# Kernel tuning notes

Measured on AMD Instinct MI355X. Metric: run time of the kernel, lower is better.

## Reference

```python
import jax, jax.numpy as jnp
import numpy as np
import math

B, H, L = 8, 256, 4096
C = 1            # channels
D_STATE = 64
DD = D_STATE // 2  # d = 32
DT_MIN, DT_MAX = 1e-3, 1e-1


def setup_inputs() -> dict:
    key = jax.random.key(0)
    ks = jax.random.split(key, 6)
    u = jax.random.normal(ks[0], (B, H, L), dtype=jnp.float32)
    # analytic init matching the torch module
    h_scale = jnp.exp(jnp.arange(H, dtype=jnp.float32) / H * math.log(DT_MAX / DT_MIN))  # (H,)
    angles = jnp.arange(DD, dtype=jnp.float32) * jnp.float32(np.pi)                      # (DD,)
    theta = jnp.einsum('c,h,d->chd', jnp.ones((C,), jnp.float32), h_scale, angles)       # (C,H,DD)
    a = -jnp.broadcast_to(h_scale[None, :, None], (C, H, DD)).astype(jnp.float32)        # (C,H,DD)
    D = jax.random.normal(ks[1], (C, H), dtype=jnp.float32)
    b_p = jax.random.normal(ks[2], (C, H, DD), dtype=jnp.float32)
    c_p = jax.random.normal(ks[3], (C, H, DD), dtype=jnp.float32)
    x0 = jax.random.normal(ks[4], (C, H, DD), dtype=jnp.float32)
    return {"u": u, "theta": theta, "a": a, "D": D, "b_p": b_p, "c_p": c_p, "x0": x0}


def fft_conv(u, f):
    # u: (B,H,L), f: (C,H,L) -> (B,C,H,L) causal conv via zero-padded FFT
    l = u.shape[-1]
    n = 2 * l
    u_f = jnp.fft.rfft(u, n=n)          # (B,H,n//2+1)
    f_f = jnp.fft.rfft(f, n=n)          # (C,H,n//2+1)
    y_f = jnp.einsum('bhl,chl->bchl', u_f, f_f)
    return jnp.fft.irfft(y_f, n=n)[..., :l]


def reference(u, theta, a, D, b_p, c_p, x0):
    l = u.shape[-1]
    T = 1.0 / (l - 1)
    zk = T * jnp.arange(l, dtype=jnp.float32)            # (L,)
    zk4 = zk[None, None, :, None]                         # (1,1,L,1)
    ls = -jnp.abs(a) + 1j * theta                         # (C,H,DD) complex
    term_0 = (jnp.exp(ls * T) - 1.0) / ls                 # (C,H,DD)
    # base_term: (C,H,L,DD)
    base_term = (2.0 * term_0[:, :, None, :] * jnp.exp(ls[:, :, None, :] * zk4)).real
    q = b_p * c_p                                         # (C,H,DD)
    f = jnp.einsum('chd,chld->chl', q, base_term)         # (C,H,L)
    y = fft_conv(u, f)                                    # (B,C,H,L)
    y = y + jnp.einsum('bhl,ch->bchl', u, D)
    # initial-condition term
    cos_term = 2.0 * T * jnp.exp(-jnp.abs(a)[:, :, None, :] * zk4) * jnp.cos(theta[:, :, None, :] * zk4)
    init = jnp.einsum('chd,chld->chl', 2.0 * (c_p * x0), cos_term)  # (C,H,L)
    y = y + init[None]                                    # broadcast over batch
    b = y.shape[0]
    return y.reshape(b, -1, l)                            # (B, C*H, L)
```

## Files before the change

kernel.cpp:

```cpp
#include <hip/hip_runtime.h>

#define BB 8
#define HH 256
#define LL 4096
#define DD2 32
#define STR 72
#define ESTR 65

typedef __attribute__((ext_vector_type(8))) short short8;
typedef __attribute__((ext_vector_type(4))) float f32x4;

static __device__ inline unsigned short f2bf(float x) {
    union { float f; unsigned u; } v; v.f = x;
    unsigned r = v.u + 0x7fffu + ((v.u >> 16) & 1u);
    return (unsigned short)(r >> 16);
}

#define CMUL(or_, oi_, ar_, ai_, br_, bi_) do { \
    float _tr = fmaf((ar_), (br_), -(ai_) * (bi_)); \
    float _ti = fmaf((ar_), (bi_), (ai_) * (br_)); \
    (or_) = _tr; (oi_) = _ti; } while (0)

__global__ __launch_bounds__(256) void s4_mfma_kernel(
    const float* __restrict__ u,
    const float* __restrict__ theta,
    const float* __restrict__ a,
    const float* __restrict__ Dp,
    const float* __restrict__ b_p,
    const float* __restrict__ c_p,
    const float* __restrict__ x0,
    float* __restrict__ out)
{
    const int tid = threadIdx.x;
    const int bh  = blockIdx.x;
    const int hh  = bh & (HH - 1);
    const float T = 1.0f / (LL - 1);

    __shared__ __align__(16) short lds[18432 + 128];
    short* Us = lds;
    short* Hs = lds + 4608;
    short* Ps = lds + 9216;
    short* Rs = lds + 13824;
    float* h_s = (float*)&lds[18432];
    float* Es  = (float*)&lds[4608];

    const float* up = u + ((size_t)bh << 12);
    #pragma unroll
    for (int jj = 0; jj < 4; ++jj) {
        const int v  = tid + (jj << 8);
        const float4 val = ((const float4*)up)[v];
        const int c  = v >> 4;
        const int t0 = (v & 15) << 2;
        uint2 pk;
        pk.x = (unsigned)f2bf(val.x) | ((unsigned)f2bf(val.y) << 16);
        pk.y = (unsigned)f2bf(val.z) | ((unsigned)f2bf(val.w) << 16);
        *(uint2*)&Us[c * STR + t0] = pk;
    }

    const int d  = tid & 31;
    const int kb = tid >> 5;
    const float lr = a[hh * DD2 + d];
    const float li = theta[hh * DD2 + d];
    float sn, cS;
    sincosf(li * T, &sn, &cS);
    const float er = expf(lr * T);
    const float Rr = er * cS, Ri = er * sn;
    const float den = lr * lr + li * li;
    const float t0r = ((Rr - 1.f) * lr + Ri * li) / den;
    const float t0i = (Ri * lr - (Rr - 1.f) * li) / den;
    const float qq  = b_p[hh * DD2 + d] * c_p[hh * DD2 + d];
    const float wre = 2.f * qq * t0r, wim = 2.f * qq * t0i;
    const float vv  = 4.f * T * c_p[hh * DD2 + d] * x0[hh * DD2 + d];

    float r2r, r2i, r4r, r4i, r8r, r8i, r16r, r16i, r32r, r32i;
    CMUL(r2r, r2i, Rr, Ri, Rr, Ri);
    CMUL(r4r, r4i, r2r, r2i, r2r, r2i);
    CMUL(r8r, r8i, r4r, r4i, r4r, r4i);
    CMUL(r16r, r16i, r8r, r8i, r8r, r8i);
    CMUL(r32r, r32i, r16r, r16i, r16r, r16i);

    float pr = 1.f, pi = 0.f;
    if (kb & 1) CMUL(pr, pi, pr, pi, r8r, r8i);
    if (kb & 2) CMUL(pr, pi, pr, pi, r16r, r16i);
    if (kb & 4) CMUL(pr, pi, pr, pi, r32r, r32i);

    #pragma unroll
    for (int k8 = 0; k8 < 8; ++k8) {
        const int k = (kb << 3) + k8;
        Rs[k * STR + d]       = (short)f2bf(pr);
        Rs[k * STR + 32 + d]  = (short)f2bf(-pi);
        Ps[d * STR + (63 - k)]        = (short)f2bf(pr);
        Ps[(32 + d) * STR + (63 - k)] = (short)f2bf(pi);
        float hk = fmaf(wre, pr, -wim * pi);
        hk += __shfl_xor(hk, 1);
        hk += __shfl_xor(hk, 2);
        hk += __shfl_xor(hk, 4);
        hk += __shfl_xor(hk, 8);
        hk += __shfl_xor(hk, 16);
        if (d == 0) h_s[k] = hk;
        CMUL(pr, pi, pr, pi, Rr, Ri);
    }
    __syncthreads();

    {
        const int t  = tid >> 2;
        const int tb = (tid & 3) << 4;
        #pragma unroll
        for (int g = 0; g < 4; ++g) {
            const int tau0 = tb + (g << 2);
            unsigned short e[4];
            #pragma unroll
            for (int i = 0; i < 4; ++i) {
                const int dt = t - (tau0 + i);
                e[i] = (dt >= 0) ? f2bf(h_s[dt]) : (unsigned short)0;
            }
            uint2 pk;
            pk.x = (unsigned)e[0] | ((unsigned)e[1] << 16);
            pk.y = (unsigned)e[2] | ((unsigned)e[3] << 16);
            *(uint2*)&Hs[t * STR + tau0] = pk;
        }
    }
    __syncthreads();

    const int ln   = tid & 63;
    const int m0   = (tid >> 6) << 4;
    const int rowi = ln & 15;
    const int quad = ln >> 4;
    f32x4 accY[4], accE[4];
    #pragma unroll
    for (int nt = 0; nt < 4; ++nt) {
        accY[nt] = (f32x4){0.f, 0.f, 0.f, 0.f};
        accE[nt] = (f32x4){0.f, 0.f, 0.f, 0.f};
    }
    #pragma unroll
    for (int k0 = 0; k0 < 64; k0 += 32) {
        const short8 aH = *(const short8*)&Hs[(m0 + rowi) * STR + k0 + (quad << 3)];
        const short8 aP = *(const short8*)&Ps[(m0 + rowi) * STR + k0 + (quad << 3)];
        #pragma unroll
        for (int nt = 0; nt < 4; ++nt) {
            const short8 bU = *(const short8*)&Us[((nt << 4) + rowi) * STR + k0 + (quad << 3)];
            accY[nt] = __builtin_amdgcn_mfma_f32_16x16x32_bf16(aH, bU, accY[nt], 0, 0, 0);
            accE[nt] = __builtin_amdgcn_mfma_f32_16x16x32_bf16(aP, bU, accE[nt], 0, 0, 0);
        }
    }
    __syncthreads();

    #pragma unroll
    for (int nt = 0; nt < 4; ++nt)
        #pragma unroll
        for (int i = 0; i < 4; ++i)
            Es[(m0 + (quad << 2) + i) * ESTR + (nt << 4) + rowi] = accE[nt][i];
    __syncthreads();

    if (tid < 32) {
        float Sr = 0.f, Si = 0.f;
        float Gr = vv, Gi = 0.f;
        float Ar, Ai;
        CMUL(Ar, Ai, r32r, r32i, r32r, r32i);
        float wrrR, wrrI;
        CMUL(wrrR, wrrI, wre, wim, Rr, Ri);
        short* Qs = Us;
        for (int c = 0; c < 64; ++c) {
            const float Er = Es[d * ESTR + c];
            const float Ei = Es[(32 + d) * ESTR + c];
            const float Qr = fmaf(wrrR, Sr, fmaf(-wrrI, Si, Gr));
            const float Qi = fmaf(wrrR, Si, fmaf(wrrI, Sr, Gi));
            Qs[c * STR + d]      = (short)f2bf(Qr);
            Qs[c * STR + 32 + d] = (short)f2bf(Qi);
            const float nSr = fmaf(Ar, Sr, fmaf(-Ai, Si, Er));
            const float nSi = fmaf(Ar, Si, fmaf(Ai, Sr, Ei));
            Sr = nSr; Si = nSi;
            float nGr, nGi;
            CMUL(nGr, nGi, Ar, Ai, Gr, Gi);
            Gr = nGr; Gi = nGi;
        }
    }
    __syncthreads();

    #pragma unroll
    for (int k0 = 0; k0 < 64; k0 += 32) {
        const short8 aR = *(const short8*)&Rs[(m0 + rowi) * STR + k0 + (quad << 3)];
        #pragma unroll
        for (int nt = 0; nt < 4; ++nt) {
            const short8 bQ = *(const short8*)&Us[((nt << 4) + rowi) * STR + k0 + (quad << 3)];
            accY[nt] = __builtin_amdgcn_mfma_f32_16x16x32_bf16(aR, bQ, accY[nt], 0, 0, 0);
        }
    }

    const float Dh = Dp[hh];
    float* op = out + ((size_t)bh << 12);
    #pragma unroll
    for (int nt = 0; nt < 4; ++nt) {
        const int c    = (nt << 4) + rowi;
        const int toff = m0 + (quad << 2);
        const float4 uu = *(const float4*)&up[c * 64 + toff];
        float4 res;
        res.x = fmaf(Dh, uu.x, accY[nt][0]);
        res.y = fmaf(Dh, uu.y, accY[nt][1]);
        res.z = fmaf(Dh, uu.z, accY[nt][2]);
        res.w = fmaf(Dh, uu.w, accY[nt][3]);
        *(float4*)&op[c * 64 + toff] = res;
    }
}

extern "C" void kernel_launch(void* const* d_in, const int* in_sizes, int n_in,
                              void* d_out, int out_size, void* d_ws, size_t ws_size,
                              hipStream_t stream) {
    const float* u     = (const float*)d_in[0];
    const float* theta = (const float*)d_in[1];
    const float* a     = (const float*)d_in[2];
    const float* Dp    = (const float*)d_in[3];
    const float* b_p   = (const float*)d_in[4];
    const float* c_p   = (const float*)d_in[5];
    const float* x0    = (const float*)d_in[6];
    float* out = (float*)d_out;
    hipLaunchKernelGGL(s4_mfma_kernel, dim3(BB * HH), dim3(256), 0, stream,
                       u, theta, a, Dp, b_p, c_p, x0, out);
}
```

Measured before the change: 110.8 us.

## Parallelize chunk-state scan across all threads and shrink LDS footprint

The serial 64-step inter-chunk recurrence, which previously ran on only 32 threads, becomes a two-level scan. Each of 8 thread groups scans 8 chunks, segment sums are combined with powers of A, and each group then emits its own Q rows. The E buffer is stored as bf16 and aliased with the H buffer, and the R matrix is built later into the P region. Together these cut LDS to about 30KB, and launch bounds now request 5 blocks per CU. The u reload is also hoisted before the final MFMA, at the cost of extra bf16 rounding in the scan state and a few more syncs.

```diff
diff --git a/kernel.cpp b/kernel.cpp
--- a/kernel.cpp
+++ b/kernel.cpp
@@ -5,7 +5,8 @@
 #define LL 4096
 #define DD2 32
 #define STR 72
-#define ESTR 65
+#define ESTRS 140
+#define SEGSTR 18
 
 typedef __attribute__((ext_vector_type(8))) short short8;
 typedef __attribute__((ext_vector_type(4))) float f32x4;
@@ -15,13 +16,16 @@
     unsigned r = v.u + 0x7fffu + ((v.u >> 16) & 1u);
     return (unsigned short)(r >> 16);
 }
+static __device__ inline float bf2f(unsigned us) {
+    union { unsigned u; float f; } v; v.u = us << 16; return v.f;
+}
 
 #define CMUL(or_, oi_, ar_, ai_, br_, bi_) do { \
     float _tr = fmaf((ar_), (br_), -(ai_) * (bi_)); \
     float _ti = fmaf((ar_), (bi_), (ai_) * (br_)); \
     (or_) = _tr; (oi_) = _ti; } while (0)
 
-__global__ __launch_bounds__(256) void s4_mfma_kernel(
+__global__ __launch_bounds__(256, 5) void s4_mfma_kernel(
     const float* __restrict__ u,
     const float* __restrict__ theta,
     const float* __restrict__ a,
@@ -36,13 +40,14 @@
     const int hh  = bh & (HH - 1);
     const float T = 1.0f / (LL - 1);
 
-    __shared__ __align__(16) short lds[18432 + 128];
-    short* Us = lds;
-    short* Hs = lds + 4608;
-    short* Ps = lds + 9216;
-    short* Rs = lds + 13824;
-    float* h_s = (float*)&lds[18432];
-    float* Es  = (float*)&lds[4608];
+    __shared__ __align__(16) short lds[15104];
+    short* Us  = lds;
+    short* Hs  = lds + 4608;
+    short* EsS = lds + 4608;
+    short* Ps  = lds + 9216;
+    short* Rs  = lds + 9216;
+    float* h_s = (float*)&lds[13824];
+    float* SegF = (float*)&lds[13952];
 
     const float* up = u + ((size_t)bh << 12);
     #pragma unroll
@@ -79,26 +84,25 @@
     CMUL(r16r, r16i, r8r, r8i, r8r, r8i);
     CMUL(r32r, r32i, r16r, r16i, r16r, r16i);
 
-    float pr = 1.f, pi = 0.f;
-    if (kb & 1) CMUL(pr, pi, pr, pi, r8r, r8i);
-    if (kb & 2) CMUL(pr, pi, pr, pi, r16r, r16i);
-    if (kb & 4) CMUL(pr, pi, pr, pi, r32r, r32i);
-
-    #pragma unroll
-    for (int k8 = 0; k8 < 8; ++k8) {
-        const int k = (kb << 3) + k8;
-        Rs[k * STR + d]       = (short)f2bf(pr);
-        Rs[k * STR + 32 + d]  = (short)f2bf(-pi);
-        Ps[d * STR + (63 - k)]        = (short)f2bf(pr);
-        Ps[(32 + d) * STR + (63 - k)] = (short)f2bf(pi);
-        float hk = fmaf(wre, pr, -wim * pi);
-        hk += __shfl_xor(hk, 1);
-        hk += __shfl_xor(hk, 2);
-        hk += __shfl_xor(hk, 4);
-        hk += __shfl_xor(hk, 8);
-        hk += __shfl_xor(hk, 16);
-        if (d == 0) h_s[k] = hk;
-        CMUL(pr, pi, pr, pi, Rr, Ri);
+    {
+        float pr = 1.f, pi = 0.f;
+        if (kb & 1) CMUL(pr, pi, pr, pi, r8r, r8i);
+        if (kb & 2) CMUL(pr, pi, pr, pi, r16r, r16i);
+        if (kb & 4) CMUL(pr, pi, pr, pi, r32r, r32i);
+        #pragma unroll
+        for (int k8 = 0; k8 < 8; ++k8) {
+            const int k = (kb << 3) + k8;
+            Ps[d * STR + (63 - k)]        = (short)f2bf(pr);
+            Ps[(32 + d) * STR + (63 - k)] = (short)f2bf(pi);
+            float hk = fmaf(wre, pr, -wim * pi);
+            hk += __shfl_xor(hk, 1);
+            hk += __shfl_xor(hk, 2);
+            hk += __shfl_xor(hk, 4);
+            hk += __shfl_xor(hk, 8);
+            hk += __shfl_xor(hk, 16);
+            if (d == 0) h_s[k] = hk;
+            CMUL(pr, pi, pr, pi, Rr, Ri);
+        }
     }
     __syncthreads();
 
@@ -148,28 +152,83 @@
     #pragma unroll
     for (int nt = 0; nt < 4; ++nt)
         #pragma unroll
-        for (int i = 0; i < 4; ++i)
-            Es[(m0 + (quad << 2) + i) * ESTR + (nt << 4) + rowi] = accE[nt][i];
-    __syncthreads();
-
-    if (tid < 32) {
+        for (int i = 0; i < 4; ++i) {
+            const int dd = m0 + (quad << 2) + i;
+            EsS[(dd & 31) * ESTRS + (((nt << 4) + rowi) << 1) + (dd >> 5)] =
+                (short)f2bf(accE[nt][i]);
+        }
+    {
+        float pr = 1.f, pi = 0.f;
+        if (kb & 1) CMUL(pr, pi, pr, pi, r8r, r8i);
+        if (kb & 2) CMUL(pr, pi, pr, pi, r16r, r16i);
+        if (kb & 4) CMUL(pr, pi, pr, pi, r32r, r32i);
+        #pragma unroll
+        for (int k8 = 0; k8 < 8; ++k8) {
+            const int k = (kb << 3) + k8;
+            Rs[k * STR + d]      = (short)f2bf(pr);
+            Rs[k * STR + 32 + d] = (short)f2bf(-pi);
+            CMUL(pr, pi, pr, pi, Rr, Ri);
+        }
+    }
+    __syncthreads();
+
+    const int g = kb;
+    float Ar, Ai;
+    CMUL(Ar, Ai, r32r, r32i, r32r, r32i);
+    {
         float Sr = 0.f, Si = 0.f;
+        #pragma unroll
+        for (int i = 0; i < 8; ++i) {
+            const unsigned ee = *(const unsigned*)&EsS[d * ESTRS + (((g << 3) + i) << 1)];
+            const float Er = bf2f(ee & 0xffffu), Ei = bf2f(ee >> 16);
+            const float nr = fmaf(Ar, Sr, fmaf(-Ai, Si, Er));
+            const float ni = fmaf(Ar, Si, fmaf(Ai, Sr, Ei));
+            Sr = nr; Si = ni;
+        }
+        SegF[d * SEGSTR + (g << 1)]     = Sr;
+        SegF[d * SEGSTR + (g << 1) + 1] = Si;
+    }
+    __syncthreads();
+
+    {
+        float S8r, S8i, S16r, S16i, S32r, S32i;
+        float b1r, b1i, b2r, b2i;
+        CMUL(b1r, b1i, Ar, Ai, Ar, Ai);
+        CMUL(b2r, b2i, b1r, b1i, b1r, b1i);
+        CMUL(S8r, S8i, b2r, b2i, b2r, b2i);
+        CMUL(S16r, S16i, S8r, S8i, S8r, S8i);
+        CMUL(S32r, S32i, S16r, S16i, S16r, S16i);
+        float offr = 0.f, offi = 0.f;
+        #pragma unroll
+        for (int gp = 0; gp < 7; ++gp) {
+            const float sr = SegF[d * SEGSTR + (gp << 1)];
+            const float si = SegF[d * SEGSTR + (gp << 1) + 1];
+            const float nr = fmaf(S8r, offr, fmaf(-S8i, offi, sr));
+            const float ni = fmaf(S8r, offi, fmaf(S8i, offr, si));
+            const bool take = gp < g;
+            offr = take ? nr : offr;
+            offi = take ? ni : offi;
+        }
         float Gr = vv, Gi = 0.f;
-        float Ar, Ai;
-        CMUL(Ar, Ai, r32r, r32i, r32r, r32i);
+        if (g & 1) { float nr, ni; CMUL(nr, ni, Gr, Gi, S8r, S8i);  Gr = nr; Gi = ni; }
+        if (g & 2) { float nr, ni; CMUL(nr, ni, Gr, Gi, S16r, S16i); Gr = nr; Gi = ni; }
+        if (g & 4) { float nr, ni; CMUL(nr, ni, Gr, Gi, S32r, S32i); Gr = nr; Gi = ni; }
         float wrrR, wrrI;
         CMUL(wrrR, wrrI, wre, wim, Rr, Ri);
+        float Sr = offr, Si = offi;
         short* Qs = Us;
-        for (int c = 0; c < 64; ++c) {
-            const float Er = Es[d * ESTR + c];
-            const float Ei = Es[(32 + d) * ESTR + c];
+        #pragma unroll
+        for (int i = 0; i < 8; ++i) {
+            const int c = (g << 3) + i;
+            const unsigned ee = *(const unsigned*)&EsS[d * ESTRS + (c << 1)];
+            const float Er = bf2f(ee & 0xffffu), Ei = bf2f(ee >> 16);
             const float Qr = fmaf(wrrR, Sr, fmaf(-wrrI, Si, Gr));
             const float Qi = fmaf(wrrR, Si, fmaf(wrrI, Sr, Gi));
             Qs[c * STR + d]      = (short)f2bf(Qr);
             Qs[c * STR + 32 + d] = (short)f2bf(Qi);
-            const float nSr = fmaf(Ar, Sr, fmaf(-Ai, Si, Er));
-            const float nSi = fmaf(Ar, Si, fmaf(Ai, Sr, Ei));
-            Sr = nSr; Si = nSi;
+            const float nr = fmaf(Ar, Sr, fmaf(-Ai, Si, Er));
+            const float ni = fmaf(Ar, Si, fmaf(Ai, Sr, Ei));
+            Sr = nr; Si = ni;
             float nGr, nGi;
             CMUL(nGr, nGi, Ar, Ai, Gr, Gi);
             Gr = nGr; Gi = nGi;
@@ -177,6 +236,11 @@
     }
     __syncthreads();
 
+    float4 uu[4];
+    #pragma unroll
+    for (int nt = 0; nt < 4; ++nt)
+        uu[nt] = *(const float4*)&up[((nt << 4) + rowi) * 64 + m0 + (quad << 2)];
+
     #pragma unroll
     for (int k0 = 0; k0 < 64; k0 += 32) {
         const short8 aR = *(const short8*)&Rs[(m0 + rowi) * STR + k0 + (quad << 3)];
@@ -193,12 +257,11 @@
     for (int nt = 0; nt < 4; ++nt) {
         const int c    = (nt << 4) + rowi;
         const int toff = m0 + (quad << 2);
-        const float4 uu = *(const float4*)&up[c * 64 + toff];
         float4 res;
-        res.x = fmaf(Dh, uu.x, accY[nt][0]);
-        res.y = fmaf(Dh, uu.y, accY[nt][1]);
-        res.z = fmaf(Dh, uu.z, accY[nt][2]);
-        res.w = fmaf(Dh, uu.w, accY[nt][3]);
+        res.x = fmaf(Dh, uu[nt].x, accY[nt][0]);
+        res.y = fmaf(Dh, uu[nt].y, accY[nt][1]);
+        res.z = fmaf(Dh, uu[nt].z, accY[nt][2]);
+        res.w = fmaf(Dh, uu[nt].w, accY[nt][3]);
         *(float4*)&op[c * 64 + toff] = res;
     }
 }
```

Result: faster. 104.9 us (-5.4%).
